# Optimization experiments

Hardware: AMD Instinct MI355X
Metric: run time of the kernel (lower is better)

## Reference

```python
import jax, jax.numpy as jnp
import numpy as np

KERNEL_SIZE = 5

def setup_inputs() -> dict:
    key = jax.random.key(0)
    k1, k2, k3 = jax.random.split(key, 3)
    H = W = 4096
    stdv = 1.0 / KERNEL_SIZE
    return {
        "input": jax.random.normal(k1, (H, W), dtype=jnp.float32),
        "K_hit": jax.random.uniform(k2, (KERNEL_SIZE, KERNEL_SIZE), dtype=jnp.float32, minval=-stdv, maxval=stdv),
        "K_miss": jax.random.uniform(k3, (KERNEL_SIZE, KERNEL_SIZE), dtype=jnp.float32, minval=-stdv, maxval=stdv),
    }

def _hitmiss(x, K_hit, K_miss):
    k = K_hit.shape[0]
    c = (k - 1) // 2
    Hout = x.shape[0] - 2 * c
    Wout = x.shape[1] - 2 * c
    # Fmap[i,j] = min_{di,dj}(x[i+di, j+dj] - K_hit[di,dj]) - max_{di,dj}(x[i+di, j+dj] - K_miss[di,dj])
    mn = jnp.full((Hout, Wout), jnp.inf, dtype=x.dtype)
    mx = jnp.full((Hout, Wout), -jnp.inf, dtype=x.dtype)
    for di in range(k):          # small fixed k*k loop over structuring-element offsets
        for dj in range(k):
            w = x[di:di + Hout, dj:dj + Wout]
            mn = jnp.minimum(mn, w - K_hit[di, dj])
            mx = jnp.maximum(mx, w - K_miss[di, dj])
    return mn - mx

def reference(input, K_hit, K_miss):
    return _hitmiss(input, K_hit, K_miss)
```

## Files before the change

kernel.cpp:

```cpp
#include <hip/hip_runtime.h>
#include <math.h>


constexpr int KS  = 5;
constexpr int WW  = 4096;
constexpr int HO  = 4092;
constexpr int WO  = 4092;
constexpr int CG  = WO / 4;
constexpr int RPT = 4;

__device__ __forceinline__ float min3f(float a, float b, float c) {
    float d;
    asm("v_min3_f32 %0, %1, %2, %3" : "=v"(d) : "v"(a), "v"(b), "v"(c));
    return d;
}
__device__ __forceinline__ float max3f(float a, float b, float c) {
    float d;
    asm("v_max3_f32 %0, %1, %2, %3" : "=v"(d) : "v"(a), "v"(b), "v"(c));
    return d;
}

__global__ __launch_bounds__(256) void hitmiss_kernel(
    const float* __restrict__ x,
    const float* __restrict__ kh,
    const float* __restrict__ km,
    float* __restrict__ out)
{
    const int cg = blockIdx.x * blockDim.x + threadIdx.x;
    if (cg >= CG) return;
    const int j0 = cg * 4;
    const int r0 = blockIdx.y * RPT;

    float wh[KS * KS], wm[KS * KS];
#pragma unroll
    for (int i = 0; i < KS * KS; ++i) {
        wh[i] = kh[i];
        wm[i] = km[i];
    }

    const float* base = x + (size_t)r0 * WW + j0;

    float mn[RPT][4], mx[RPT][4];

#pragma unroll
    for (int i = 0; i < RPT + 4; ++i) {
        float4 a = *reinterpret_cast<const float4*>(base + (size_t)i * WW);
        float4 b = *reinterpret_cast<const float4*>(base + (size_t)i * WW + 4);
        const float v[8] = {a.x, a.y, a.z, a.w, b.x, b.y, b.z, b.w};

#pragma unroll
        for (int o = 0; o < RPT; ++o) {
            const int di = i - o;
            if (di < 0 || di > KS - 1) continue;
#pragma unroll
            for (int p = 0; p < 4; ++p) {
                const float t0 = v[p + 0] - wh[di * KS + 0];
                const float t1 = v[p + 1] - wh[di * KS + 1];
                const float t2 = v[p + 2] - wh[di * KS + 2];
                const float t3 = v[p + 3] - wh[di * KS + 3];
                const float t4 = v[p + 4] - wh[di * KS + 4];
                const float m5 = min3f(t3, t4, min3f(t0, t1, t2));
                mn[o][p] = (di == 0) ? m5 : fminf(mn[o][p], m5);

                const float u0 = v[p + 0] - wm[di * KS + 0];
                const float u1 = v[p + 1] - wm[di * KS + 1];
                const float u2 = v[p + 2] - wm[di * KS + 2];
                const float u3 = v[p + 3] - wm[di * KS + 3];
                const float u4 = v[p + 4] - wm[di * KS + 4];
                const float x5 = max3f(u3, u4, max3f(u0, u1, u2));
                mx[o][p] = (di == 0) ? x5 : fmaxf(mx[o][p], x5);
            }
        }

        if (i >= KS - 1) {
            const int o = i - (KS - 1);
            float4 oo;
            oo.x = mn[o][0] - mx[o][0];
            oo.y = mn[o][1] - mx[o][1];
            oo.z = mn[o][2] - mx[o][2];
            oo.w = mn[o][3] - mx[o][3];
            *reinterpret_cast<float4*>(out + (size_t)(r0 + o) * WO + j0) = oo;
        }
    }
}

extern "C" void kernel_launch(void* const* d_in, const int* in_sizes, int n_in,
                              void* d_out, int out_size, void* d_ws, size_t ws_size,
                              hipStream_t stream) {
    const float* x  = (const float*)d_in[0];
    const float* kh = (const float*)d_in[1];
    const float* km = (const float*)d_in[2];
    float* out = (float*)d_out;

    dim3 block(256, 1, 1);
    dim3 grid((CG + 255) / 256, HO / RPT, 1);
    hipLaunchKernelGGL(hitmiss_kernel, grid, block, 0, stream, x, kh, km, out);
}
```

Baseline: 126.6 us.

## Use packed v_pk_add_f32 subtraction with shifted unaligned loads and min3 accumulation

Kernel weights are negated once so each subtraction becomes an add. Pairs of output columns are then computed with two-wide float vectors, which lets the compiler emit packed f32 adds. An extra unaligned load at offset +1 supplies the odd-shifted pairs so no lane shuffling is needed. The accumulator is folded into a min3/max3 to shorten the reduction chain, and launch bounds now request 8 blocks per CU. The extra loads add memory traffic, which is mostly absorbed by cache, and the occupancy hint may force register spills.

Measured after the change: 250.6 us. +97.9%, slower.

```diff
diff --git a/kernel.cpp b/kernel.cpp
--- a/kernel.cpp
+++ b/kernel.cpp
@@ -8,6 +8,11 @@
 constexpr int WO  = 4092;
 constexpr int CG  = WO / 4;
 constexpr int RPT = 4;
+
+typedef float v2f  __attribute__((ext_vector_type(2)));
+typedef float f4a4 __attribute__((ext_vector_type(4), aligned(4)));
+typedef float f2a4 __attribute__((ext_vector_type(2), aligned(4)));
+typedef float f4a16 __attribute__((ext_vector_type(4), aligned(16)));
 
 __device__ __forceinline__ float min3f(float a, float b, float c) {
     float d;
@@ -20,7 +25,20 @@
     return d;
 }
 
-__global__ __launch_bounds__(256) void hitmiss_kernel(
+__device__ __forceinline__ float red5_min(float t0, float t1, float t2, float t3, float t4) {
+    return min3f(min3f(t0, t1, t2), t3, t4);
+}
+__device__ __forceinline__ float red5_max(float t0, float t1, float t2, float t3, float t4) {
+    return max3f(max3f(t0, t1, t2), t3, t4);
+}
+__device__ __forceinline__ float red5acc_min(float acc, float t0, float t1, float t2, float t3, float t4) {
+    return fminf(min3f(t0, t1, t2), min3f(t3, t4, acc));
+}
+__device__ __forceinline__ float red5acc_max(float acc, float t0, float t1, float t2, float t3, float t4) {
+    return fmaxf(max3f(t0, t1, t2), max3f(t3, t4, acc));
+}
+
+__global__ __launch_bounds__(256, 8) void hitmiss_kernel(
     const float* __restrict__ x,
     const float* __restrict__ kh,
     const float* __restrict__ km,
@@ -31,11 +49,11 @@
     const int j0 = cg * 4;
     const int r0 = blockIdx.y * RPT;
 
-    float wh[KS * KS], wm[KS * KS];
+    float nh[KS * KS], nm[KS * KS];
 #pragma unroll
-    for (int i = 0; i < KS * KS; ++i) {
-        wh[i] = kh[i];
-        wm[i] = km[i];
+    for (int k = 0; k < KS * KS; ++k) {
+        nh[k] = -kh[k];
+        nm[k] = -km[k];
     }
 
     const float* base = x + (size_t)r0 * WW + j0;
@@ -44,31 +62,53 @@
 
 #pragma unroll
     for (int i = 0; i < RPT + 4; ++i) {
-        float4 a = *reinterpret_cast<const float4*>(base + (size_t)i * WW);
-        float4 b = *reinterpret_cast<const float4*>(base + (size_t)i * WW + 4);
-        const float v[8] = {a.x, a.y, a.z, a.w, b.x, b.y, b.z, b.w};
+        const float* rp = base + (size_t)i * WW;
+        f4a16 a0 = *reinterpret_cast<const f4a16*>(rp);
+        f4a16 a1 = *reinterpret_cast<const f4a16*>(rp + 4);
+        f4a4  b0 = *reinterpret_cast<const f4a4 *>(rp + 1);
+        f2a4  b1 = *reinterpret_cast<const f2a4 *>(rp + 5);
+
+        const v2f A0 = {a0.x, a0.y}, A1 = {a0.z, a0.w};
+        const v2f A2 = {a1.x, a1.y}, A3 = {a1.z, a1.w};
+        const v2f B0 = {b0.x, b0.y}, B1 = {b0.z, b0.w};
+        const v2f B2 = {b1.x, b1.y};
+
+        const v2f p01[KS] = {A0, B0, A1, B1, A2};
+        const v2f p23[KS] = {A1, B1, A2, B2, A3};
 
 #pragma unroll
         for (int o = 0; o < RPT; ++o) {
             const int di = i - o;
             if (di < 0 || di > KS - 1) continue;
+            const int kb = di * KS;
+
+            v2f th01[KS], tm01[KS], th23[KS], tm23[KS];
 #pragma unroll
-            for (int p = 0; p < 4; ++p) {
-                const float t0 = v[p + 0] - wh[di * KS + 0];
-                const float t1 = v[p + 1] - wh[di * KS + 1];
-                const float t2 = v[p + 2] - wh[di * KS + 2];
-                const float t3 = v[p + 3] - wh[di * KS + 3];
-                const float t4 = v[p + 4] - wh[di * KS + 4];
-                const float m5 = min3f(t3, t4, min3f(t0, t1, t2));
-                mn[o][p] = (di == 0) ? m5 : fminf(mn[o][p], m5);
+            for (int j = 0; j < KS; ++j) {
+                th01[j] = p01[j] + nh[kb + j];
+                tm01[j] = p01[j] + nm[kb + j];
+                th23[j] = p23[j] + nh[kb + j];
+                tm23[j] = p23[j] + nm[kb + j];
+            }
 
-                const float u0 = v[p + 0] - wm[di * KS + 0];
-                const float u1 = v[p + 1] - wm[di * KS + 1];
-                const float u2 = v[p + 2] - wm[di * KS + 2];
-                const float u3 = v[p + 3] - wm[di * KS + 3];
-                const float u4 = v[p + 4] - wm[di * KS + 4];
-                const float x5 = max3f(u3, u4, max3f(u0, u1, u2));
-                mx[o][p] = (di == 0) ? x5 : fmaxf(mx[o][p], x5);
+            if (di == 0) {
+                mn[o][0] = red5_min(th01[0].x, th01[1].x, th01[2].x, th01[3].x, th01[4].x);
+                mn[o][1] = red5_min(th01[0].y, th01[1].y, th01[2].y, th01[3].y, th01[4].y);
+                mn[o][2] = red5_min(th23[0].x, th23[1].x, th23[2].x, th23[3].x, th23[4].x);
+                mn[o][3] = red5_min(th23[0].y, th23[1].y, th23[2].y, th23[3].y, th23[4].y);
+                mx[o][0] = red5_max(tm01[0].x, tm01[1].x, tm01[2].x, tm01[3].x, tm01[4].x);
+                mx[o][1] = red5_max(tm01[0].y, tm01[1].y, tm01[2].y, tm01[3].y, tm01[4].y);
+                mx[o][2] = red5_max(tm23[0].x, tm23[1].x, tm23[2].x, tm23[3].x, tm23[4].x);
+                mx[o][3] = red5_max(tm23[0].y, tm23[1].y, tm23[2].y, tm23[3].y, tm23[4].y);
+            } else {
+                mn[o][0] = red5acc_min(mn[o][0], th01[0].x, th01[1].x, th01[2].x, th01[3].x, th01[4].x);
+                mn[o][1] = red5acc_min(mn[o][1], th01[0].y, th01[1].y, th01[2].y, th01[3].y, th01[4].y);
+                mn[o][2] = red5acc_min(mn[o][2], th23[0].x, th23[1].x, th23[2].x, th23[3].x, th23[4].x);
+                mn[o][3] = red5acc_min(mn[o][3], th23[0].y, th23[1].y, th23[2].y, th23[3].y, th23[4].y);
+                mx[o][0] = red5acc_max(mx[o][0], tm01[0].x, tm01[1].x, tm01[2].x, tm01[3].x, tm01[4].x);
+                mx[o][1] = red5acc_max(mx[o][1], tm01[0].y, tm01[1].y, tm01[2].y, tm01[3].y, tm01[4].y);
+                mx[o][2] = red5acc_max(mx[o][2], tm23[0].x, tm23[1].x, tm23[2].x, tm23[3].x, tm23[4].x);
+                mx[o][3] = red5acc_max(mx[o][3], tm23[0].y, tm23[1].y, tm23[2].y, tm23[3].y, tm23[4].y);
             }
         }
 
```
